# Kernel tuning notes

Measured on AMD Instinct MI355X. Metric: run time of the kernel, lower is better.

## Reference

```python
import jax, jax.numpy as jnp
import numpy as np

N_NODES = 100000
N_EDGES = 1600000
N_GRAPHS = 512


def _init_linear(key, fan_in, fan_out):
    kw, kb = jax.random.split(key)
    scale = 1.0 / np.sqrt(fan_in)
    W = jax.random.normal(kw, (fan_in, fan_out), dtype=jnp.float32) * scale
    b = jax.random.normal(kb, (fan_out,), dtype=jnp.float32) * 0.01
    return W, b


def setup_inputs() -> dict:
    key = jax.random.key(0)
    ks = jax.random.split(key, 9)
    x = jax.random.normal(ks[0], (N_NODES, 2), dtype=jnp.float32)
    edge_index = jax.random.randint(ks[1], (2, N_EDGES), 0, N_NODES, dtype=jnp.int64)
    batch = jnp.sort(jax.random.randint(ks[2], (N_NODES,), 0, N_GRAPHS, dtype=jnp.int64))
    dims = [(2, 16), (16, 32), (32, 64), (64, 128), (128, 64), (64, 10)]
    params = {}
    for i, (fi, fo) in enumerate(dims):
        W, b = _init_linear(ks[3 + i], fi, fo)
        params[f"W{i+1}"] = W
        params[f"b{i+1}"] = b
    return dict(x=x, edge_index=edge_index, batch=batch, **params)


def _gcn_layer(x, src, dst, norm, W, b):
    # message = norm * x[src]; aggregate by sum over destination node
    msg = x[src] * norm[:, None]                        # [E+N, C]
    agg = jax.ops.segment_sum(msg, dst, num_segments=N_NODES)  # [N, C]
    return jax.nn.relu(agg @ W + b)


def reference(x, edge_index, batch, W1, b1, W2, b2, W3, b3, W4, b4, W5, b5, W6, b6):
    # GCN with added self-loops and symmetric normalization D^-1/2 A_hat D^-1/2
    self_idx = jnp.arange(N_NODES, dtype=edge_index.dtype)
    src = jnp.concatenate([edge_index[0], self_idx])
    dst = jnp.concatenate([edge_index[1], self_idx])
    deg = jax.ops.segment_sum(jnp.ones_like(dst, dtype=x.dtype), dst, num_segments=N_NODES)
    deg_isqrt = jax.lax.rsqrt(deg)                      # deg >= 1 via self-loops
    norm = deg_isqrt[src] * deg_isqrt[dst]

    h = _gcn_layer(x, src, dst, norm, W1, b1)           # [N, 16]
    h = _gcn_layer(h, src, dst, norm, W2, b2)           # [N, 32]
    h = _gcn_layer(h, src, dst, norm, W3, b3)           # [N, 64]
    h = _gcn_layer(h, src, dst, norm, W4, b4)           # [N, 128]

    # scatter_max graph pooling over batch assignment
    pooled = jax.ops.segment_max(h, batch, num_segments=N_GRAPHS)  # [G, 128]
    pooled = jnp.where(jnp.isfinite(pooled), pooled, 0.0)

    h = jax.nn.relu(pooled @ W5 + b5)                   # [G, 64]
    out = h @ W6 + b6                                   # [G, 10]
    return out
```

## Files before the change

kernel.cpp:

```cpp
#include <hip/hip_runtime.h>
#include <hip/hip_fp16.h>

typedef __attribute__((ext_vector_type(4))) float f32x4;
typedef __attribute__((ext_vector_type(2))) float f32x2;
typedef __attribute__((ext_vector_type(4))) int i32x4;
typedef _Float16 f16x8 __attribute__((ext_vector_type(8)));
typedef _Float16 f16x4 __attribute__((ext_vector_type(4)));

#define EPB 4096
#define NBKT 196
#define BCAP 10240

__global__ __launch_bounds__(256)
void init_kernel(int* __restrict__ bktCur, float* __restrict__ pooled,
                 const float* __restrict__ W, _Float16* __restrict__ Wpk) {
    const int gid = blockIdx.x * 256 + threadIdx.x;
    if (gid < NBKT) bktCur[gid] = 0;
    if (gid < 512 * 128) pooled[gid] = 0.f;
    if (gid < 8192) {
        const int i = gid & 7;
        const int l = (gid >> 3) & 63;
        const int kk = (gid >> 9) & 1;
        const int ct = gid >> 10;
        const int k = kk * 32 + 4 * (l >> 4) + (i & 3) + 16 * (i >> 2);
        const int col = ct * 16 + (l & 15);
        Wpk[gid] = (_Float16)W[k * 128 + col];
    }
}

__global__ __launch_bounds__(256)
void partition_kernel(const int* __restrict__ ei, int E,
                      int* __restrict__ bktCur, int* __restrict__ arena) {
    __shared__ int sHist[256];
    __shared__ int sScan[256];
    __shared__ int sAdj[256];
    __shared__ int2 sEdges[EPB];
    const int t = threadIdx.x;
    const int e0 = blockIdx.x * EPB;
    const int ecnt = min(EPB, E - e0);
    const int* src = ei;
    const int* dst = ei + E;

    sHist[t] = 0;
    __syncthreads();
    for (int k = t; k < ecnt; k += 256) {
        const int s = src[e0 + k], d = dst[e0 + k];
        sEdges[k] = make_int2(s, d);
        atomicAdd(&sHist[d >> 9], 1);
    }
    __syncthreads();
    const int v = sHist[t];
    sScan[t] = v;
    __syncthreads();
    #pragma unroll
    for (int off = 1; off < 256; off <<= 1) {
        const int y = (t >= off) ? sScan[t - off] : 0;
        __syncthreads();
        sScan[t] += y;
        __syncthreads();
    }
    const int excl = sScan[t] - v;
    if (t < NBKT && v > 0) {
        const int g = atomicAdd(&bktCur[t], v);
        sAdj[t] = t * BCAP + g - excl;
    }
    sHist[t] = excl;
    __syncthreads();
    for (int k = t; k < ecnt; k += 256) {
        const int2 e = sEdges[k];
        const int b = e.y >> 9;
        const int p = atomicAdd(&sHist[b], 1);
        arena[sAdj[b] + p] = (e.x << 9) | (e.y & 511);
    }
}

__global__ __launch_bounds__(512)
void bucket_csr_kernel(const int* __restrict__ arena, const int* __restrict__ bktCur,
                       int* __restrict__ csr_src, int2* __restrict__ meta,
                       float* __restrict__ dis, const float* __restrict__ x,
                       float* __restrict__ g0, int n) {
    __shared__ int sHist[512];
    __shared__ int sScan[512];
    const int t = threadIdx.x;
    const int b = blockIdx.x;
    const int base = b * BCAP;
    const int cnt_b = min(bktCur[b], BCAP);

    sHist[t] = 0;
    __syncthreads();
    for (int e = t; e < cnt_b; e += 512)
        atomicAdd(&sHist[arena[base + e] & 511], 1);
    __syncthreads();
    const int v = sHist[t];
    sScan[t] = v;
    __syncthreads();
    #pragma unroll
    for (int off = 1; off < 512; off <<= 1) {
        const int y = (t >= off) ? sScan[t - off] : 0;
        __syncthreads();
        sScan[t] += y;
        __syncthreads();
    }
    const int excl = sScan[t] - v;
    const int node = b * 512 + t;
    if (node < n) {
        meta[node] = make_int2(base + excl, v);
        const float d = (float)(1.0 / sqrt((double)(v + 1)));
        dis[node] = d;
        float2 xv = *(const float2*)(x + 2 * (size_t)node);
        xv.x *= d; xv.y *= d;
        *(float2*)(g0 + 2 * (size_t)node) = xv;
    }
    sHist[t] = excl;
    __syncthreads();
    for (int e = t; e < cnt_b; e += 512) {
        const int pv = arena[base + e];
        const int p = atomicAdd(&sHist[pv & 511], 1);
        csr_src[base + p] = pv >> 9;
    }
}

__global__ __launch_bounds__(256, 6)
void gcn_l1_lane(const float* __restrict__ g0, const int2* __restrict__ meta,
                 const int* __restrict__ csr_src, const float* __restrict__ dis,
                 const float* __restrict__ W, const float* __restrict__ B,
                 __half* __restrict__ g1h, int n) {
    __shared__ float sW[32];
    __shared__ float sB[16];
    const int tid = threadIdx.x;
    if (tid < 32) sW[tid] = W[tid];
    if (tid < 16) sB[tid] = B[tid];
    __syncthreads();
    const int node = blockIdx.x * 256 + tid;
    if (node >= n) return;
    const int2 mt = meta[node];
    const int start = mt.x, m = mt.y;
    float a0 = 0.f, a1 = 0.f;
    for (int j = 0; j < m; j += 8) {
        int ss[8]; float mm[8];
        #pragma unroll
        for (int u = 0; u < 8; ++u) {
            const int jj = j + u;
            const bool ok = jj < m;
            ss[u] = csr_src[start + (ok ? jj : 0)];
            mm[u] = ok ? 1.f : 0.f;
        }
        f32x2 hv[8];
        const float* ap[8];
        #pragma unroll
        for (int u = 0; u < 8; ++u) ap[u] = g0 + 2 * (size_t)ss[u];
        #pragma unroll
        for (int u = 0; u < 8; ++u)
            asm volatile("global_load_dwordx2 %0, %1, off"
                         : "=v"(hv[u]) : "v"(ap[u]) : "memory");
        asm volatile("s_waitcnt vmcnt(0)" ::: "memory");
        __builtin_amdgcn_sched_barrier(0);
        #pragma unroll
        for (int u = 0; u < 8; ++u) {
            a0 = fmaf(mm[u], hv[u].x, a0);
            a1 = fmaf(mm[u], hv[u].y, a1);
        }
    }
    const float d0 = dis[node];
    const float2 hs = *(const float2*)(g0 + 2 * (size_t)node);
    a0 = (a0 + hs.x) * d0;
    a1 = (a1 + hs.y) * d0;
    f16x8 o0, o1;
    #pragma unroll
    for (int o = 0; o < 8; ++o) {
        const float v0 = fmaxf(fmaf(a0, sW[o], fmaf(a1, sW[16 + o], sB[o])), 0.f);
        const float v1 = fmaxf(fmaf(a0, sW[o + 8], fmaf(a1, sW[24 + o], sB[o + 8])), 0.f);
        o0[o] = (_Float16)(d0 * v0);
        o1[o] = (_Float16)(d0 * v1);
    }
    *(f16x8*)((_Float16*)g1h + (size_t)node * 16) = o0;
    *(f16x8*)((_Float16*)g1h + (size_t)node * 16 + 8) = o1;
}

template <int C_IN, bool OUT_HALF>
__global__ __launch_bounds__(256, 6)
void agg_group_kernel(const __half* __restrict__ g_in, const int2* __restrict__ meta,
                      const int* __restrict__ csr_src, const float* __restrict__ dis,
                      void* __restrict__ agg_v, int n) {
    constexpr int LPR = C_IN / 8;
    constexpr int GPW = 64 / LPR;

    const int lane = threadIdx.x & 63;
    const int wv = threadIdx.x >> 6;
    const int grp = lane / LPR;
    const int sl  = lane % LPR;
    const int node = ((size_t)blockIdx.x * 4 + wv) * GPW + grp;
    const bool valid = node < n;

    const int2 mt = valid ? meta[node] : make_int2(0, 0);
    const int start = mt.x, m = mt.y;
    const int cb = sl * 8;

    float a[8];
    #pragma unroll
    for (int q = 0; q < 8; ++q) a[q] = 0.f;

    for (int j = 0; j < m; j += 8) {
        int ss[8]; float mm[8];
        #pragma unroll
        for (int u = 0; u < 8; ++u) {
            const int jj = j + u;
            const bool ok = jj < m;
            ss[u] = csr_src[start + (ok ? jj : 0)];
            mm[u] = ok ? 1.f : 0.f;
        }
        i32x4 hr[8];
        const __half* ap[8];
        #pragma unroll
        for (int u = 0; u < 8; ++u) ap[u] = g_in + (size_t)ss[u] * C_IN + cb;
        #pragma unroll
        for (int u = 0; u < 8; ++u)
            asm volatile("global_load_dwordx4 %0, %1, off"
                         : "=v"(hr[u]) : "v"(ap[u]) : "memory");
        asm volatile("s_waitcnt vmcnt(0)" ::: "memory");
        __builtin_amdgcn_sched_barrier(0);
        #pragma unroll
        for (int u = 0; u < 8; ++u) {
            #pragma unroll
            for (int q = 0; q < 4; ++q) {
                const int wbits = hr[u][q];
                const __half2 h2 = *(const __half2*)&wbits;
                const float2 f2 = __half22float2(h2);
                a[2 * q]     = fmaf(mm[u], f2.x, a[2 * q]);
                a[2 * q + 1] = fmaf(mm[u], f2.y, a[2 * q + 1]);
            }
        }
    }

    if (valid) {
        const float d0 = dis[node];
        const __half* hp = g_in + (size_t)node * C_IN + cb;
        #pragma unroll
        for (int q = 0; q < 4; ++q) {
            const __half2 h2 = *(const __half2*)(hp + 2 * q);
            const float2 f2 = __half22float2(h2);
            a[2 * q]     = (a[2 * q]     + f2.x) * d0;
            a[2 * q + 1] = (a[2 * q + 1] + f2.y) * d0;
        }
        if constexpr (OUT_HALF) {
            f16x8 t;
            #pragma unroll
            for (int q = 0; q < 8; ++q) t[q] = (_Float16)a[q];
            *(f16x8*)((_Float16*)agg_v + (size_t)node * C_IN + cb) = t;
        } else {
            float* agg = (float*)agg_v;
            f32x4 t0, t1;
            t0.x = a[0]; t0.y = a[1]; t0.z = a[2]; t0.w = a[3];
            t1.x = a[4]; t1.y = a[5]; t1.z = a[6]; t1.w = a[7];
            *(f32x4*)&agg[(size_t)node * C_IN + cb] = t0;
            *(f32x4*)&agg[(size_t)node * C_IN + cb + 4] = t1;
        }
    }
}

template <int C_IN, int C_OUT, bool OUT_HALF>
__global__ __launch_bounds__(256, 3)
void gemm_kernel(const float* __restrict__ agg, const float* __restrict__ W,
                 const float* __restrict__ Bias, const float* __restrict__ dis,
                 void* __restrict__ g_out_v, int n) {
    constexpr int QW = C_OUT / 16;
    constexpr int RPT = QW;
    constexpr int LOGQ = (QW == 8) ? 3 : (QW == 4) ? 2 : 1;
    constexpr int CH = C_IN / 4;
    constexpr int SA = 68;

    constexpr int W_BYTES = C_IN * C_OUT * 4 + C_OUT * 4;
    constexpr int R1 = (W_BYTES + 15) & ~15;
    constexpr int AT_BYTES = C_IN * SA * 4;
    __shared__ char smem[R1 + AT_BYTES];
    __shared__ float sDis[64];

    float* sW = (float*)smem;
    float* sB = sW + C_IN * C_OUT;
    float* sAt = (float*)(smem + R1);

    const int tid = threadIdx.x;
    const int base = blockIdx.x * 64;

    for (int i = tid; i < C_IN * C_OUT / 4; i += 256)
        ((f32x4*)sW)[i] = ((const f32x4*)W)[i];
    if (tid < C_OUT) sB[tid] = Bias[tid];
    {
        constexpr int RPP = 256 / CH;
        const int r = tid / CH, c0 = tid % CH;
        #pragma unroll
        for (int p = 0; p < 64 / RPP; ++p) {
            const int rr = p * RPP + r;
            const int node = base + rr;
            f32x4 v = {0.f, 0.f, 0.f, 0.f};
            if (node < n) v = *(const f32x4*)&agg[(size_t)node * C_IN + c0 * 4];
            sAt[(c0 * 4 + 0) * SA + rr] = v.x;
            sAt[(c0 * 4 + 1) * SA + rr] = v.y;
            sAt[(c0 * 4 + 2) * SA + rr] = v.z;
            sAt[(c0 * 4 + 3) * SA + rr] = v.w;
        }
    }
    if (tid < 64) sDis[tid] = (base + tid < n) ? dis[base + tid] : 0.f;
    __syncthreads();

    const int w = tid >> 6, l = tid & 63;
    const int j = l & (QW - 1);
    const int rg = l >> LOGQ;
    const int ob = w * (C_OUT / 4) + j * 4;

    f32x4 acc[RPT];
    {
        const f32x4 bv = *(const f32x4*)&sB[ob];
        #pragma unroll
        for (int r = 0; r < RPT; ++r) acc[r] = bv;
    }

    #pragma unroll 4
    for (int k = 0; k < C_IN; ++k) {
        const f32x4 wv = ((const f32x4*)sW)[k * (C_OUT / 4) + (ob >> 2)];
        float av[RPT];
        if constexpr (RPT == 4) {
            const f32x4 a0 = *(const f32x4*)&sAt[k * SA + rg * 4];
            av[0] = a0.x; av[1] = a0.y; av[2] = a0.z; av[3] = a0.w;
        } else {
            const float2 a0 = *(const float2*)&sAt[k * SA + rg * 2];
            av[0] = a0.x; av[1] = a0.y;
        }
        #pragma unroll
        for (int r = 0; r < RPT; ++r) {
            acc[r].x = fmaf(av[r], wv.x, acc[r].x);
            acc[r].y = fmaf(av[r], wv.y, acc[r].y);
            acc[r].z = fmaf(av[r], wv.z, acc[r].z);
            acc[r].w = fmaf(av[r], wv.w, acc[r].w);
        }
    }

    #pragma unroll
    for (int r = 0; r < RPT; ++r) {
        const int row = rg * RPT + r;
        const int node = base + row;
        if (node < n) {
            const float sd = sDis[row];
            const float o0 = sd * fmaxf(acc[r].x, 0.f);
            const float o1 = sd * fmaxf(acc[r].y, 0.f);
            const float o2 = sd * fmaxf(acc[r].z, 0.f);
            const float o3 = sd * fmaxf(acc[r].w, 0.f);
            if constexpr (OUT_HALF) {
                __half2 lo = __floats2half2_rn(o0, o1);
                __half2 hi = __floats2half2_rn(o2, o3);
                uint2 pk;
                pk.x = *(unsigned int*)&lo;
                pk.y = *(unsigned int*)&hi;
                *(uint2*)((__half*)g_out_v + (size_t)node * C_OUT + ob) = pk;
            } else {
                f32x4 o; o.x = o0; o.y = o1; o.z = o2; o.w = o3;
                *(f32x4*)((float*)g_out_v + (size_t)node * C_OUT + ob) = o;
            }
        }
    }
}

__global__ __launch_bounds__(256, 6)
void fused_layer3(const __half* __restrict__ g2h, const int2* __restrict__ meta,
                  const int* __restrict__ csr_src, const float* __restrict__ dis,
                  const float* __restrict__ W, const float* __restrict__ Bias,
                  __half* __restrict__ g3h, int n) {
    constexpr int SA = 68;
    __shared__ float sW[32 * 64];
    __shared__ float sB[64];
    __shared__ float sAt[32 * SA];
    __shared__ float sDis[64];

    const int tid = threadIdx.x;
    const int base = blockIdx.x * 64;
    const int lane = tid & 63, wv = tid >> 6;

    for (int i = tid; i < 32 * 64 / 4; i += 256)
        ((f32x4*)sW)[i] = ((const f32x4*)W)[i];
    if (tid < 64) sB[tid] = Bias[tid];
    if (tid < 64) sDis[tid] = (base + tid < n) ? dis[base + tid] : 0.f;

    {
        const int row = wv * 16 + (lane >> 2);
        const int sl = lane & 3;
        const int cb = sl * 8;
        const int node = base + row;
        const bool valid = node < n;
        const int2 mt = valid ? meta[node] : make_int2(0, 0);
        const int start = mt.x, m = mt.y;

        float a[8];
        #pragma unroll
        for (int q = 0; q < 8; ++q) a[q] = 0.f;

        for (int j = 0; j < m; j += 8) {
            int ss[8]; float mm[8];
            #pragma unroll
            for (int u = 0; u < 8; ++u) {
                const int jj = j + u;
                const bool ok = jj < m;
                ss[u] = csr_src[start + (ok ? jj : 0)];
                mm[u] = ok ? 1.f : 0.f;
            }
            i32x4 hr[8];
            const __half* ap[8];
            #pragma unroll
            for (int u = 0; u < 8; ++u) ap[u] = g2h + (size_t)ss[u] * 32 + cb;
            #pragma unroll
            for (int u = 0; u < 8; ++u)
                asm volatile("global_load_dwordx4 %0, %1, off"
                             : "=v"(hr[u]) : "v"(ap[u]) : "memory");
            asm volatile("s_waitcnt vmcnt(0)" ::: "memory");
            __builtin_amdgcn_sched_barrier(0);
            #pragma unroll
            for (int u = 0; u < 8; ++u) {
                #pragma unroll
                for (int q = 0; q < 4; ++q) {
                    const int wbits = hr[u][q];
                    const __half2 h2 = *(const __half2*)&wbits;
                    const float2 f2 = __half22float2(h2);
                    a[2 * q]     = fmaf(mm[u], f2.x, a[2 * q]);
                    a[2 * q + 1] = fmaf(mm[u], f2.y, a[2 * q + 1]);
                }
            }
        }
        float d0 = 0.f;
        if (valid) {
            d0 = dis[node];
            const __half* hp = g2h + (size_t)node * 32 + cb;
            #pragma unroll
            for (int q = 0; q < 4; ++q) {
                const __half2 h2 = *(const __half2*)(hp + 2 * q);
                const float2 f2 = __half22float2(h2);
                a[2 * q]     = (a[2 * q]     + f2.x) * d0;
                a[2 * q + 1] = (a[2 * q + 1] + f2.y) * d0;
            }
        }
        #pragma unroll
        for (int q = 0; q < 8; ++q)
            sAt[(cb + q) * SA + row] = valid ? a[q] : 0.f;
    }
    __syncthreads();

    const int j = lane & 3;
    const int rg = lane >> 2;
    const int ob = wv * 16 + j * 4;

    f32x4 acc[4];
    {
        const f32x4 bv = *(const f32x4*)&sB[ob];
        #pragma unroll
        for (int r = 0; r < 4; ++r) acc[r] = bv;
    }
    #pragma unroll 4
    for (int k = 0; k < 32; ++k) {
        const f32x4 wvv = ((const f32x4*)sW)[k * 16 + (ob >> 2)];
        const f32x4 a0 = *(const f32x4*)&sAt[k * SA + rg * 4];
        float av[4] = {a0.x, a0.y, a0.z, a0.w};
        #pragma unroll
        for (int r = 0; r < 4; ++r) {
            acc[r].x = fmaf(av[r], wvv.x, acc[r].x);
            acc[r].y = fmaf(av[r], wvv.y, acc[r].y);
            acc[r].z = fmaf(av[r], wvv.z, acc[r].z);
            acc[r].w = fmaf(av[r], wvv.w, acc[r].w);
        }
    }
    #pragma unroll
    for (int r = 0; r < 4; ++r) {
        const int row = rg * 4 + r;
        const int node = base + row;
        if (node < n) {
            const float sd = sDis[row];
            __half2 lo = __floats2half2_rn(sd * fmaxf(acc[r].x, 0.f), sd * fmaxf(acc[r].y, 0.f));
            __half2 hi = __floats2half2_rn(sd * fmaxf(acc[r].z, 0.f), sd * fmaxf(acc[r].w, 0.f));
            uint2 pk;
            pk.x = *(unsigned int*)&lo;
            pk.y = *(unsigned int*)&hi;
            *(uint2*)((__half*)g3h + (size_t)node * 64 + ob) = pk;
        }
    }
}

__global__ __launch_bounds__(256, 4)
void fused_layer4(const __half* __restrict__ g3h, const int2* __restrict__ meta,
                  const int* __restrict__ csr_src, const float* __restrict__ dis,
                  const _Float16* __restrict__ Wpk, const float* __restrict__ Bias,
                  const int* __restrict__ batchv, float* __restrict__ pooled, int n) {
    constexpr int SA = 68;
    constexpr int AT_BYTES = 64 * SA * 4;
    constexpr int P_BYTES = 4 * 16 * 132 * 4;
    __shared__ char smem[(AT_BYTES > P_BYTES ? AT_BYTES : P_BYTES)];
    __shared__ int sGb[64];
    float* sAt = (float*)smem;
    float* sP = (float*)smem;

    const int tid = threadIdx.x;
    const int lane = tid & 63, wv = tid >> 6;
    const int base = blockIdx.x * 64;

    if (tid < 64) sGb[tid] = (base + tid < n) ? batchv[base + tid] : -1;

    {
        const int grp = wv * 8 + (lane >> 3);
        const int sl = lane & 7;
        const int cb = sl * 8;
        #pragma unroll 1
        for (int rr = 0; rr < 2; ++rr) {
            const int row = grp + rr * 32;
            const int node = base + row;
            const bool valid = node < n;
            const int2 mt = valid ? meta[node] : make_int2(0, 0);
            const int start = mt.x, m = mt.y;

            float a[8];
            #pragma unroll
            for (int q = 0; q < 8; ++q) a[q] = 0.f;

            for (int j = 0; j < m; j += 8) {
                int ss[8]; float mm[8];
                #pragma unroll
                for (int u = 0; u < 8; ++u) {
                    const int jj = j + u;
                    const bool ok = jj < m;
                    ss[u] = csr_src[start + (ok ? jj : 0)];
                    mm[u] = ok ? 1.f : 0.f;
                }
                i32x4 hr[8];
                const __half* ap[8];
                #pragma unroll
                for (int u = 0; u < 8; ++u) ap[u] = g3h + (size_t)ss[u] * 64 + cb;
                #pragma unroll
                for (int u = 0; u < 8; ++u)
                    asm volatile("global_load_dwordx4 %0, %1, off"
                                 : "=v"(hr[u]) : "v"(ap[u]) : "memory");
                asm volatile("s_waitcnt vmcnt(0)" ::: "memory");
                __builtin_amdgcn_sched_barrier(0);
                #pragma unroll
                for (int u = 0; u < 8; ++u) {
                    #pragma unroll
                    for (int q = 0; q < 4; ++q) {
                        const int wbits = hr[u][q];
                        const __half2 h2 = *(const __half2*)&wbits;
                        const float2 f2 = __half22float2(h2);
                        a[2 * q]     = fmaf(mm[u], f2.x, a[2 * q]);
                        a[2 * q + 1] = fmaf(mm[u], f2.y, a[2 * q + 1]);
                    }
                }
            }
            float d0 = 0.f;
            if (valid) {
                d0 = dis[node];
                const __half* hp = g3h + (size_t)node * 64 + cb;
                #pragma unroll
                for (int q = 0; q < 4; ++q) {
                    const __half2 h2 = *(const __half2*)(hp + 2 * q);
                    const float2 f2 = __half22float2(h2);
                    a[2 * q]     = (a[2 * q]     + f2.x) * d0;
                    a[2 * q + 1] = (a[2 * q + 1] + f2.y) * d0;
                }
            }
            #pragma unroll
            for (int q = 0; q < 8; ++q)
                sAt[(cb + q) * SA + row] = valid ? a[q] : 0.f;
        }
    }
    __syncthreads();

    const int row_a = wv * 16 + (lane & 15);
    const int kb = lane >> 4;
    f16x8 a0, a1;
    #pragma unroll
    for (int i = 0; i < 8; ++i) {
        const int k0 = 4 * kb + (i & 3) + 16 * (i >> 2);
        const int k1 = 32 + k0;
        a0[i] = (_Float16)sAt[k0 * SA + row_a];
        a1[i] = (_Float16)sAt[k1 * SA + row_a];
    }
    __syncthreads();

    f32x4 acc[8];
    #pragma unroll
    for (int ct = 0; ct < 8; ++ct) {
        f32x4 z = {0.f, 0.f, 0.f, 0.f};
        const f16x8 b0 = *(const f16x8*)(Wpk + ((ct * 2 + 0) * 64 + lane) * 8);
        const f16x8 b1 = *(const f16x8*)(Wpk + ((ct * 2 + 1) * 64 + lane) * 8);
        z = __builtin_amdgcn_mfma_f32_16x16x32_f16(a0, b0, z, 0, 0, 0);
        z = __builtin_amdgcn_mfma_f32_16x16x32_f16(a1, b1, z, 0, 0, 0);
        acc[ct] = z;
    }

    #pragma unroll
    for (int ct = 0; ct < 8; ++ct) {
        const float b = Bias[ct * 16 + (lane & 15)];
        #pragma unroll
        for (int r = 0; r < 4; ++r) {
            const int mrow = (lane >> 4) * 4 + r;
            sP[(wv * 16 + mrow) * 132 + ct * 16 + (lane & 15)] = fmaxf(acc[ct][r] + b, 0.f);
        }
    }
    __syncthreads();

    if (tid < 128) {
        const int c = tid;
        int curg = -1; float run = 0.f;
        for (int r2 = 0; r2 < 64; ++r2) {
            const int gb = sGb[r2];
            if (gb < 0) continue;
            const float v = sP[r2 * 132 + c];
            if (gb != curg) {
                if (curg >= 0)
                    atomicMax((int*)&pooled[(size_t)curg * 128 + c], __float_as_int(run));
                curg = gb; run = v;
            } else {
                run = fmaxf(run, v);
            }
        }
        if (curg >= 0)
            atomicMax((int*)&pooled[(size_t)curg * 128 + c], __float_as_int(run));
    }
}

__global__ void mlp_kernel(const float* __restrict__ pooled,
                           const float* __restrict__ W5, const float* __restrict__ b5,
                           const float* __restrict__ W6, const float* __restrict__ b6,
                           float* __restrict__ out) {
    const int g = blockIdx.x;
    const int t = threadIdx.x;
    __shared__ float row[128];
    __shared__ float hid[64];
    row[t] = pooled[g * 128 + t];
    row[64 + t] = pooled[g * 128 + 64 + t];
    __syncthreads();
    float v = b5[t];
    #pragma unroll 8
    for (int c = 0; c < 128; ++c) v = fmaf(row[c], W5[c * 64 + t], v);
    hid[t] = fmaxf(v, 0.f);
    __syncthreads();
    if (t < 10) {
        float o = b6[t];
        #pragma unroll 8
        for (int c = 0; c < 64; ++c) o = fmaf(hid[c], W6[c * 10 + t], o);
        out[g * 10 + t] = o;
    }
}

extern "C" void kernel_launch(void* const* d_in, const int* in_sizes, int n_in,
                              void* d_out, int out_size, void* d_ws, size_t ws_size,
                              hipStream_t stream) {
    const float* x     = (const float*)d_in[0];
    const int*   ei    = (const int*)d_in[1];
    const int*   batch = (const int*)d_in[2];
    const float* W1 = (const float*)d_in[3];  const float* b1 = (const float*)d_in[4];
    const float* W2 = (const float*)d_in[5];  const float* b2 = (const float*)d_in[6];
    const float* W3 = (const float*)d_in[7];  const float* b3 = (const float*)d_in[8];
    const float* W4 = (const float*)d_in[9];  const float* b4 = (const float*)d_in[10];
    const float* W5 = (const float*)d_in[11]; const float* b5 = (const float*)d_in[12];
    const float* W6 = (const float*)d_in[13]; const float* b6 = (const float*)d_in[14];
    float* out = (float*)d_out;

    const int N = in_sizes[0] / 2;
    const int E = in_sizes[1] / 2;
    const int G = out_size / 10;

    char* p = (char*)d_ws;
    auto take = [&](size_t bytes) -> void* {
        void* r = (void*)p;
        p += (bytes + 255) & ~(size_t)255;
        return r;
    };
    int*       bktCur = (int*)take(NBKT * 4);
    int*       arena  = (int*)take((size_t)NBKT * BCAP * 4);
    int*       csr_src= (int*)take((size_t)NBKT * BCAP * 4);
    float*     dis    = (float*)take((size_t)N * 4);
    int2*      meta   = (int2*)take((size_t)N * 8);
    float*     g0     = (float*)take((size_t)N * 2 * 4);
    __half*    g1h    = (__half*)take((size_t)N * 16 * 2);
    __half*    g2h    = (__half*)take((size_t)N * 32 * 2);
    __half*    g3h    = (__half*)take((size_t)N * 64 * 2);
    float*     aggb   = (float*)take((size_t)N * 16 * 4);
    _Float16*  Wpk    = (_Float16*)take(8192 * 2);
    float*     pooled = (float*)take((size_t)G * 128 * 4);

    init_kernel<<<(512 * 128 + 255) / 256, 256, 0, stream>>>(bktCur, pooled, W4, Wpk);

    const int PBLK = (E + EPB - 1) / EPB;
    partition_kernel<<<PBLK, 256, 0, stream>>>(ei, E, bktCur, arena);
    bucket_csr_kernel<<<NBKT, 512, 0, stream>>>(arena, bktCur, csr_src, meta, dis, x, g0, N);

    gcn_l1_lane<<<(N + 255) / 256, 256, 0, stream>>>(g0, meta, csr_src, dis, W1, b1, g1h, N);

    const int GBLK = (N + 63) / 64;

    agg_group_kernel<16, false><<<(N + 127) / 128, 256, 0, stream>>>(g1h, meta, csr_src, dis, aggb, N);
    gemm_kernel<16, 32, true><<<GBLK, 256, 0, stream>>>(aggb, W2, b2, dis, g2h, N);

    fused_layer3<<<GBLK, 256, 0, stream>>>(g2h, meta, csr_src, dis, W3, b3, g3h, N);
    fused_layer4<<<GBLK, 256, 0, stream>>>(g3h, meta, csr_src, dis, Wpk, b4, batch, pooled, N);

    mlp_kernel<<<G, 64, 0, stream>>>(pooled, W5, b5, W6, b6, out);
}
```

Baseline: 169.7 us.

## Split layer-4 into separate aggregation kernel and MFMA GEMM-pool kernel

Replaces the fused layer-4 kernel, which gathered neighbours and then ran the MFMA GEMM with max-pooling, with two kernels. The first is a reusable agg_group_kernel<64,true> that writes aggregated fp16 rows to a new buffer. The second is an MFMA GEMM that loads A fragments straight from global memory. The intent is to give the gather phase better occupancy and parallelism, since it no longer shares register and LDS budgets with the GEMM. The cost is an extra N×64 fp16 round trip through global memory and one more kernel launch.

New measurement: 173.3 us. 2.1% more time.

```diff
diff --git a/kernel.cpp b/kernel.cpp
--- a/kernel.cpp
+++ b/kernel.cpp
@@ -481,109 +481,36 @@
     }
 }
 
-__global__ __launch_bounds__(256, 4)
-void fused_layer4(const __half* __restrict__ g3h, const int2* __restrict__ meta,
-                  const int* __restrict__ csr_src, const float* __restrict__ dis,
-                  const _Float16* __restrict__ Wpk, const float* __restrict__ Bias,
-                  const int* __restrict__ batchv, float* __restrict__ pooled, int n) {
-    constexpr int SA = 68;
-    constexpr int AT_BYTES = 64 * SA * 4;
-    constexpr int P_BYTES = 4 * 16 * 132 * 4;
-    __shared__ char smem[(AT_BYTES > P_BYTES ? AT_BYTES : P_BYTES)];
+__global__ __launch_bounds__(256)
+void gemm4_mfma_kernel(const _Float16* __restrict__ aggh, const _Float16* __restrict__ Wpk,
+                       const float* __restrict__ Bias, const int* __restrict__ batchv,
+                       float* __restrict__ pooled, int n) {
+    __shared__ float sP[4][16][132];
     __shared__ int sGb[64];
-    float* sAt = (float*)smem;
-    float* sP = (float*)smem;
 
     const int tid = threadIdx.x;
-    const int lane = tid & 63, wv = tid >> 6;
+    const int w = tid >> 6, l = tid & 63;
     const int base = blockIdx.x * 64;
 
     if (tid < 64) sGb[tid] = (base + tid < n) ? batchv[base + tid] : -1;
 
-    {
-        const int grp = wv * 8 + (lane >> 3);
-        const int sl = lane & 7;
-        const int cb = sl * 8;
-        #pragma unroll 1
-        for (int rr = 0; rr < 2; ++rr) {
-            const int row = grp + rr * 32;
-            const int node = base + row;
-            const bool valid = node < n;
-            const int2 mt = valid ? meta[node] : make_int2(0, 0);
-            const int start = mt.x, m = mt.y;
-
-            float a[8];
-            #pragma unroll
-            for (int q = 0; q < 8; ++q) a[q] = 0.f;
-
-            for (int j = 0; j < m; j += 8) {
-                int ss[8]; float mm[8];
-                #pragma unroll
-                for (int u = 0; u < 8; ++u) {
-                    const int jj = j + u;
-                    const bool ok = jj < m;
-                    ss[u] = csr_src[start + (ok ? jj : 0)];
-                    mm[u] = ok ? 1.f : 0.f;
-                }
-                i32x4 hr[8];
-                const __half* ap[8];
-                #pragma unroll
-                for (int u = 0; u < 8; ++u) ap[u] = g3h + (size_t)ss[u] * 64 + cb;
-                #pragma unroll
-                for (int u = 0; u < 8; ++u)
-                    asm volatile("global_load_dwordx4 %0, %1, off"
-                                 : "=v"(hr[u]) : "v"(ap[u]) : "memory");
-                asm volatile("s_waitcnt vmcnt(0)" ::: "memory");
-                __builtin_amdgcn_sched_barrier(0);
-                #pragma unroll
-                for (int u = 0; u < 8; ++u) {
-                    #pragma unroll
-                    for (int q = 0; q < 4; ++q) {
-                        const int wbits = hr[u][q];
-                        const __half2 h2 = *(const __half2*)&wbits;
-                        const float2 f2 = __half22float2(h2);
-                        a[2 * q]     = fmaf(mm[u], f2.x, a[2 * q]);
-                        a[2 * q + 1] = fmaf(mm[u], f2.y, a[2 * q + 1]);
-                    }
-                }
-            }
-            float d0 = 0.f;
-            if (valid) {
-                d0 = dis[node];
-                const __half* hp = g3h + (size_t)node * 64 + cb;
-                #pragma unroll
-                for (int q = 0; q < 4; ++q) {
-                    const __half2 h2 = *(const __half2*)(hp + 2 * q);
-                    const float2 f2 = __half22float2(h2);
-                    a[2 * q]     = (a[2 * q]     + f2.x) * d0;
-                    a[2 * q + 1] = (a[2 * q + 1] + f2.y) * d0;
-                }
-            }
-            #pragma unroll
-            for (int q = 0; q < 8; ++q)
-                sAt[(cb + q) * SA + row] = valid ? a[q] : 0.f;
-        }
-    }
-    __syncthreads();
-
-    const int row_a = wv * 16 + (lane & 15);
-    const int kb = lane >> 4;
-    f16x8 a0, a1;
-    #pragma unroll
-    for (int i = 0; i < 8; ++i) {
-        const int k0 = 4 * kb + (i & 3) + 16 * (i >> 2);
-        const int k1 = 32 + k0;
-        a0[i] = (_Float16)sAt[k0 * SA + row_a];
-        a1[i] = (_Float16)sAt[k1 * SA + row_a];
-    }
-    __syncthreads();
+    int node_a = base + w * 16 + (l & 15);
+    if (node_a >= n) node_a = n - 1;
+    const int kb = l >> 4;
+    const f16x4* rowp = (const f16x4*)(aggh + (size_t)node_a * 64);
+    const f16x4 a00 = rowp[kb];
+    const f16x4 a01 = rowp[4 + kb];
+    const f16x4 a10 = rowp[8 + kb];
+    const f16x4 a11 = rowp[12 + kb];
+    const f16x8 a0 = __builtin_shufflevector(a00, a01, 0, 1, 2, 3, 4, 5, 6, 7);
+    const f16x8 a1 = __builtin_shufflevector(a10, a11, 0, 1, 2, 3, 4, 5, 6, 7);
 
     f32x4 acc[8];
     #pragma unroll
     for (int ct = 0; ct < 8; ++ct) {
         f32x4 z = {0.f, 0.f, 0.f, 0.f};
-        const f16x8 b0 = *(const f16x8*)(Wpk + ((ct * 2 + 0) * 64 + lane) * 8);
-        const f16x8 b1 = *(const f16x8*)(Wpk + ((ct * 2 + 1) * 64 + lane) * 8);
+        const f16x8 b0 = *(const f16x8*)(Wpk + ((ct * 2 + 0) * 64 + l) * 8);
+        const f16x8 b1 = *(const f16x8*)(Wpk + ((ct * 2 + 1) * 64 + l) * 8);
         z = __builtin_amdgcn_mfma_f32_16x16x32_f16(a0, b0, z, 0, 0, 0);
         z = __builtin_amdgcn_mfma_f32_16x16x32_f16(a1, b1, z, 0, 0, 0);
         acc[ct] = z;
@@ -591,11 +518,11 @@
 
     #pragma unroll
     for (int ct = 0; ct < 8; ++ct) {
-        const float b = Bias[ct * 16 + (lane & 15)];
+        const float b = Bias[ct * 16 + (l & 15)];
         #pragma unroll
         for (int r = 0; r < 4; ++r) {
-            const int mrow = (lane >> 4) * 4 + r;
-            sP[(wv * 16 + mrow) * 132 + ct * 16 + (lane & 15)] = fmaxf(acc[ct][r] + b, 0.f);
+            const int m = (l >> 4) * 4 + r;
+            sP[w][m][ct * 16 + (l & 15)] = fmaxf(acc[ct][r] + b, 0.f);
         }
     }
     __syncthreads();
@@ -606,7 +533,7 @@
         for (int r2 = 0; r2 < 64; ++r2) {
             const int gb = sGb[r2];
             if (gb < 0) continue;
-            const float v = sP[r2 * 132 + c];
+            const float v = sP[r2 >> 4][r2 & 15][c];
             if (gb != curg) {
                 if (curg >= 0)
                     atomicMax((int*)&pooled[(size_t)curg * 128 + c], __float_as_int(run));
@@ -678,6 +605,7 @@
     __half*    g2h    = (__half*)take((size_t)N * 32 * 2);
     __half*    g3h    = (__half*)take((size_t)N * 64 * 2);
     float*     aggb   = (float*)take((size_t)N * 16 * 4);
+    _Float16*  aggh   = (_Float16*)take((size_t)N * 64 * 2);
     _Float16*  Wpk    = (_Float16*)take(8192 * 2);
     float*     pooled = (float*)take((size_t)G * 128 * 4);
 
@@ -695,7 +623,9 @@
     gemm_kernel<16, 32, true><<<GBLK, 256, 0, stream>>>(aggb, W2, b2, dis, g2h, N);
 
     fused_layer3<<<GBLK, 256, 0, stream>>>(g2h, meta, csr_src, dis, W3, b3, g3h, N);
-    fused_layer4<<<GBLK, 256, 0, stream>>>(g3h, meta, csr_src, dis, Wpk, b4, batch, pooled, N);
+
+    agg_group_kernel<64, true><<<(N + 31) / 32, 256, 0, stream>>>(g3h, meta, csr_src, dis, aggh, N);
+    gemm4_mfma_kernel<<<GBLK, 256, 0, stream>>>(aggh, Wpk, b4, batch, pooled, N);
 
     mlp_kernel<<<G, 64, 0, stream>>>(pooled, W5, b5, W6, b6, out);
 }
```
